# Performance work log

Hardware: AMD Instinct MI355X
Metric: run time of the kernel (lower is better)

## Reference

```python
import jax, jax.numpy as jnp
import numpy as np

B, IN_CH, OUT_CH = 4, 64, 128
N_HIGH, N_LOW = 163842, 40962
GROUPS, EPS, SLOPE = 4, 1e-5, 0.2


def setup_inputs() -> dict:
    key = jax.random.key(0)
    ks = jax.random.split(key, 6)
    x = jax.random.normal(ks[0], (B, IN_CH, N_HIGH), jnp.float32)
    pool_neigh = jax.random.randint(ks[1], (N_LOW * 7,), 0, N_HIGH, dtype=jnp.int32)
    conv_neigh = jax.random.randint(ks[2], (N_LOW * 7,), 0, N_LOW, dtype=jnp.int32)
    W1 = jax.random.normal(ks[3], (OUT_CH, 7 * IN_CH), jnp.float32) / np.float32(np.sqrt(7 * IN_CH))
    b1 = jnp.zeros((OUT_CH,), jnp.float32)
    W2 = jax.random.normal(ks[4], (OUT_CH, 7 * OUT_CH), jnp.float32) / np.float32(np.sqrt(7 * OUT_CH))
    b2 = jnp.zeros((OUT_CH,), jnp.float32)
    return dict(x=x, pool_neigh=pool_neigh, conv_neigh=conv_neigh,
                W1=W1, b1=b1, gn1_w=jnp.ones((OUT_CH,), jnp.float32), gn1_b=jnp.zeros((OUT_CH,), jnp.float32),
                W2=W2, b2=b2, gn2_w=jnp.ones((OUT_CH,), jnp.float32), gn2_b=jnp.zeros((OUT_CH,), jnp.float32))


def _mean_pool(x, pool_neigh):
    # x: (B, C, N_high); pool_neigh: (N_low*7,) -> (B, C, N_low)
    g = x[:, :, pool_neigh].reshape(x.shape[0], x.shape[1], -1, 7)
    return g.mean(axis=-1)


def _onering_conv(x, neigh, W, b):
    # x: (B, C, N); neigh: (N*7,); W: (O, 7*C). Torch Linear over gathered
    # (N*7, C).view(N, 7*C): neighbor-major, channel-minor concatenation.
    Bb, C, N = x.shape
    feat = x[:, :, neigh].reshape(Bb, C, N, 7)            # (B, C, N, 7)
    feat = jnp.transpose(feat, (0, 2, 3, 1)).reshape(Bb, N, 7 * C)  # (B, N, 7C)
    out = jnp.einsum('bnf,of->bno', feat, W) + b          # (B, N, O)
    return jnp.transpose(out, (0, 2, 1))                  # (B, O, N)


def _group_norm(x, w, b):
    # x: (B, C, N), normalize per (group, sample) over (C//G, N)
    Bb, C, N = x.shape
    xg = x.reshape(Bb, GROUPS, C // GROUPS, N)
    mu = xg.mean(axis=(2, 3), keepdims=True)
    var = ((xg - mu) ** 2).mean(axis=(2, 3), keepdims=True)
    xn = ((xg - mu) * jax.lax.rsqrt(var + EPS)).reshape(Bb, C, N)
    return xn * w[None, :, None] + b[None, :, None]


def _leaky_relu(x):
    return jnp.where(x >= 0, x, SLOPE * x)


def reference(x, pool_neigh, conv_neigh, W1, b1, gn1_w, gn1_b, W2, b2, gn2_w, gn2_b):
    h = _mean_pool(x, pool_neigh)
    h = _leaky_relu(_group_norm(_onering_conv(h, conv_neigh, W1, b1), gn1_w, gn1_b))
    h = _leaky_relu(_group_norm(_onering_conv(h, conv_neigh, W2, b2), gn2_w, gn2_b))
    return h
```

## Files before the change

### kernel.cpp

```cpp
#include <hip/hip_runtime.h>

#define B_SZ 4
#define IN_CH 64
#define OUT_CH 128
#define NHI 163842
#define NLO 40962
#define EPS_GN 1e-5f
#define SLOPE 0.2f

typedef __attribute__((ext_vector_type(8))) short short8;
typedef __attribute__((ext_vector_type(16))) float f32x16;

__device__ inline ushort f2bf(float f) {
    union { float f; unsigned u; } v; v.f = f;
    unsigned r = v.u + 0x7FFF + ((v.u >> 16) & 1);
    return (ushort)(r >> 16);
}
__device__ inline float bf2f(ushort h) {
    union { unsigned u; float f; } v; v.u = ((unsigned)h) << 16;
    return v.f;
}

__device__ inline void glds16(const ushort* g, ushort* l) {
    typedef __attribute__((address_space(1))) const void gv;
    typedef __attribute__((address_space(3))) void lv;
    __builtin_amdgcn_global_load_lds((gv*)g, (lv*)l, 16, 0, 0);
}

__global__ void k_transpose_x(const float* __restrict__ x, ushort* __restrict__ xT) {
    __shared__ float t[64][65];
    const int b   = blockIdx.y;
    const int n0  = blockIdx.x * 64;
    const int tid = threadIdx.x;
    const int nq  = tid & 15;
    const int c0  = tid >> 4;
    const bool full = (n0 + 64) <= NHI;
    if (full) {
#pragma unroll
        for (int r = 0; r < 4; ++r) {
            int c = c0 + r * 16;
            float4 v = *(const float4*)&x[((long)b * IN_CH + c) * NHI + n0 + nq * 4];
            t[c][nq * 4 + 0] = v.x; t[c][nq * 4 + 1] = v.y;
            t[c][nq * 4 + 2] = v.z; t[c][nq * 4 + 3] = v.w;
        }
    } else {
        for (int r = 0; r < 4; ++r) {
            int c = c0 + r * 16;
            for (int e = 0; e < 4; ++e) {
                int n = n0 + nq * 4 + e;
                t[c][nq * 4 + e] = (n < NHI) ? x[((long)b * IN_CH + c) * NHI + n] : 0.f;
            }
        }
    }
    __syncthreads();
    const int n  = tid >> 2;
    const int cc = (tid & 3) * 16;
    if (n0 + n < NHI) {
        short8 o0, o1;
#pragma unroll
        for (int e = 0; e < 8; ++e) {
            o0[e] = (short)f2bf(t[cc + e][n]);
            o1[e] = (short)f2bf(t[cc + 8 + e][n]);
        }
        ushort* p = &xT[((long)b * NHI + n0 + n) * 64 + cc];
        *(short8*)p = o0;
        *(short8*)(p + 8) = o1;
    }
}

__global__ void k_prep_w(const float* __restrict__ W, ushort* __restrict__ Wb, int K) {
    int i = blockIdx.x * 256 + threadIdx.x;
    if (i >= K * 128) return;
    int k = i / 128, o = i % 128;
    int step = k >> 6, kk = k & 63, kg = kk >> 3, e = kk & 7;
    Wb[(((long)(step * 8 + kg) * 128 + o) * 8) + e] = f2bf(W[(long)o * K + k]);
}

__global__ void k_pool(const ushort* __restrict__ xT, const int* __restrict__ pn,
                       ushort* __restrict__ h1) {
    long t = (long)blockIdx.x * 256 + threadIdx.x;
    const long total = (long)B_SZ * NLO * 8;
    if (t >= total) return;
    int  cq = (int)(t & 7);
    long bn = t >> 3;
    int  n  = (int)(bn % NLO);
    int  b  = (int)(bn / NLO);
    float acc[8] = {};
#pragma unroll
    for (int j = 0; j < 7; ++j) {
        int idx = pn[n * 7 + j];
        short8 v = *(const short8*)&xT[((long)b * NHI + idx) * 64 + cq * 8];
#pragma unroll
        for (int e = 0; e < 8; ++e) acc[e] += bf2f((ushort)v[e]);
    }
    short8 o;
#pragma unroll
    for (int e = 0; e < 8; ++e) o[e] = (short)f2bf(acc[e] * (1.f / 7.f));
    *(short8*)&h1[bn * 64 + cq * 8] = o;
}

template <int CIN>
__global__ __launch_bounds__(256, 2)
void k_conv_mfma(const ushort* __restrict__ src, const int* __restrict__ nbr,
                 const ushort* __restrict__ Wb, const float* __restrict__ bias,
                 ushort* __restrict__ out, float* __restrict__ part) {
    constexpr int NSTEP = 7 * CIN / 64;
    __shared__ ushort Asm[2][8192];
    __shared__ ushort Bsm[2][8192];
    __shared__ float  red[4][2][2];

    const int b     = blockIdx.y;
    const int n0    = blockIdx.x * 128;
    const int tid   = threadIdx.x;
    const int lane  = tid & 63;
    const int wave  = tid >> 6;
    const int wr    = wave >> 1, wc = wave & 1;
    const int l31   = lane & 31;
    const int khalf = lane >> 5;

    const int s_nn = tid >> 2;
    const int s_kq = tid & 3;
    const int r0 = min(n0 + s_nn, NLO - 1);
    const int r1 = min(n0 + 64 + s_nn, NLO - 1);
    int nb0[7], nb1[7];
#pragma unroll
    for (int j = 0; j < 7; ++j) {
        nb0[j] = nbr[r0 * 7 + j];
        nb1[j] = nbr[r1 * 7 + j];
    }

    const long srcb = (long)b * NLO * CIN;
    f32x16 acc[2][2] = {};
    short8 a00, a01, a10, a11;

#pragma unroll
    for (int i = 0; i < 4; ++i) {
        int off = (wave * 4 + i) * 512;
        glds16(&Wb[off + lane * 8], &Bsm[0][off]);
    }
    {
        const ushort* p0 = &src[srcb + (long)nb0[0] * CIN + s_kq * 8];
        const ushort* p1 = &src[srcb + (long)nb1[0] * CIN + s_kq * 8];
        a00 = *(const short8*)p0; a01 = *(const short8*)(p0 + 32);
        a10 = *(const short8*)p1; a11 = *(const short8*)(p1 + 32);
        *(short8*)&Asm[0][(s_kq * 128 + s_nn) * 8]            = a00;
        *(short8*)&Asm[0][((s_kq + 4) * 128 + s_nn) * 8]      = a01;
        *(short8*)&Asm[0][(s_kq * 128 + 64 + s_nn) * 8]       = a10;
        *(short8*)&Asm[0][((s_kq + 4) * 128 + 64 + s_nn) * 8] = a11;
    }
    __syncthreads();

    for (int step = 0; step < NSTEP; ++step) {
        const int cur = step & 1;
        const int nxt = cur ^ 1;
        if (step + 1 < NSTEP) {
#pragma unroll
            for (int i = 0; i < 4; ++i) {
                int off = (wave * 4 + i) * 512;
                glds16(&Wb[(long)(step + 1) * 8192 + off + lane * 8], &Bsm[nxt][off]);
            }
            const int s  = step + 1;
            const int j  = (CIN == 64) ? s : (s >> 1);
            const int cb = (CIN == 64) ? 0 : ((s & 1) * 64);
            const ushort* p0 = &src[srcb + (long)nb0[j] * CIN + cb + s_kq * 8];
            const ushort* p1 = &src[srcb + (long)nb1[j] * CIN + cb + s_kq * 8];
            a00 = *(const short8*)p0; a01 = *(const short8*)(p0 + 32);
            a10 = *(const short8*)p1; a11 = *(const short8*)(p1 + 32);
        }
#pragma unroll
        for (int kh = 0; kh < 4; ++kh) {
            const int kg = 2 * kh + khalf;
            short8 A0 = *(const short8*)&Asm[cur][(kg * 128 + wr * 64 + l31) * 8];
            short8 A1 = *(const short8*)&Asm[cur][(kg * 128 + wr * 64 + 32 + l31) * 8];
            short8 B0 = *(const short8*)&Bsm[cur][(kg * 128 + wc * 64 + l31) * 8];
            short8 B1 = *(const short8*)&Bsm[cur][(kg * 128 + wc * 64 + 32 + l31) * 8];
            acc[0][0] = __builtin_amdgcn_mfma_f32_32x32x16_bf16(A0, B0, acc[0][0], 0, 0, 0);
            acc[0][1] = __builtin_amdgcn_mfma_f32_32x32x16_bf16(A0, B1, acc[0][1], 0, 0, 0);
            acc[1][0] = __builtin_amdgcn_mfma_f32_32x32x16_bf16(A1, B0, acc[1][0], 0, 0, 0);
            acc[1][1] = __builtin_amdgcn_mfma_f32_32x32x16_bf16(A1, B1, acc[1][1], 0, 0, 0);
        }
        if (step + 1 < NSTEP) {
            *(short8*)&Asm[nxt][(s_kq * 128 + s_nn) * 8]            = a00;
            *(short8*)&Asm[nxt][((s_kq + 4) * 128 + s_nn) * 8]      = a01;
            *(short8*)&Asm[nxt][(s_kq * 128 + 64 + s_nn) * 8]       = a10;
            *(short8*)&Asm[nxt][((s_kq + 4) * 128 + 64 + s_nn) * 8] = a11;
        }
        __syncthreads();
    }

    float bia[2];
#pragma unroll
    for (int n = 0; n < 2; ++n) bia[n] = bias[wc * 64 + n * 32 + l31];
    float s[2] = {}, q[2] = {};
#pragma unroll
    for (int m = 0; m < 2; ++m)
#pragma unroll
        for (int n = 0; n < 2; ++n)
#pragma unroll
            for (int r = 0; r < 16; ++r) {
                int crow = (r & 3) + 8 * (r >> 2) + 4 * khalf;
                int row  = n0 + wr * 64 + m * 32 + crow;
                float v  = acc[m][n][r] + bia[n];
                if (row < NLO) {
                    out[((long)b * NLO + row) * 128 + wc * 64 + n * 32 + l31] = f2bf(v);
                    s[n] += v; q[n] += v * v;
                }
            }
#pragma unroll
    for (int n = 0; n < 2; ++n)
#pragma unroll
        for (int off = 32; off > 0; off >>= 1) {
            s[n] += __shfl_down(s[n], off);
            q[n] += __shfl_down(q[n], off);
        }
    if (lane == 0) {
#pragma unroll
        for (int n = 0; n < 2; ++n) { red[wave][n][0] = s[n]; red[wave][n][1] = q[n]; }
    }
    __syncthreads();
    if (tid < 8) {
        int g = tid >> 1, isq = tid & 1;
        int gwc = g >> 1, gn = g & 1;
        float v = red[gwc][gn][isq] + red[2 + gwc][gn][isq];
        part[(((long)b * gridDim.x + blockIdx.x) * 4 + g) * 2 + isq] = v;
    }
}

__global__ void k_finalize(const float* __restrict__ part, int nblk,
                           const float* __restrict__ w, const float* __restrict__ bb,
                           float* __restrict__ scale, float* __restrict__ shift) {
    const int b = blockIdx.x >> 2, g = blockIdx.x & 3;
    const int tid = threadIdx.x;
    float s = 0.f, ss = 0.f;
    for (int k = tid; k < nblk; k += 256) {
        s  += part[(((long)b * nblk + k) * 4 + g) * 2 + 0];
        ss += part[(((long)b * nblk + k) * 4 + g) * 2 + 1];
    }
#pragma unroll
    for (int off = 32; off > 0; off >>= 1) {
        s += __shfl_down(s, off); ss += __shfl_down(ss, off);
    }
    __shared__ float red[8];
    __shared__ float fin[2];
    const int wave = tid >> 6, lane = tid & 63;
    if (lane == 0) { red[wave * 2] = s; red[wave * 2 + 1] = ss; }
    __syncthreads();
    if (tid == 0) {
        float as = red[0] + red[2] + red[4] + red[6];
        float aq = red[1] + red[3] + red[5] + red[7];
        const float cnt = 32.f * NLO;
        float mu  = as / cnt;
        float var = aq / cnt - mu * mu;
        fin[0] = mu; fin[1] = rsqrtf(var + EPS_GN);
    }
    __syncthreads();
    if (tid < 32) {
        int c = g * 32 + tid;
        float sc = fin[1] * w[c];
        scale[b * 128 + c] = sc;
        shift[b * 128 + c] = bb[c] - fin[0] * sc;
    }
}

__global__ void k_gnapply(const ushort* __restrict__ y, const float* __restrict__ sc,
                          const float* __restrict__ sh, ushort* __restrict__ yp) {
    long t = (long)blockIdx.x * 256 + threadIdx.x;
    const long total = (long)B_SZ * NLO * 16;
    if (t >= total) return;
    int  c8 = (int)(t & 15);
    long bn = t >> 4;
    int  b  = (int)(bn / NLO);
    short8 v = *(const short8*)&y[bn * 128 + c8 * 8];
    short8 o;
#pragma unroll
    for (int e = 0; e < 8; ++e) {
        int c = c8 * 8 + e;
        float f = bf2f((ushort)v[e]) * sc[b * 128 + c] + sh[b * 128 + c];
        f = fmaxf(f, SLOPE * f);
        o[e] = (short)f2bf(f);
    }
    *(short8*)&yp[bn * 128 + c8 * 8] = o;
}

__global__ void k_output(const ushort* __restrict__ y2, const float* __restrict__ scale,
                         const float* __restrict__ shift, float* __restrict__ out) {
    __shared__ float t[32][129];
    const int b   = blockIdx.y;
    const int n0  = blockIdx.x * 32;
    const int tid = threadIdx.x;
    const float* scb = &scale[b * 128];
    const float* shb = &shift[b * 128];
    const int c8 = (tid & 15) * 8;
#pragma unroll
    for (int r = 0; r < 2; ++r) {
        int nn = (tid >> 4) + r * 16;
        int n  = n0 + nn;
        if (n < NLO) {
            short8 v = *(const short8*)&y2[((long)b * NLO + n) * 128 + c8];
#pragma unroll
            for (int e = 0; e < 8; ++e) {
                int c = c8 + e;
                float f = bf2f((ushort)v[e]) * scb[c] + shb[c];
                t[nn][c] = fmaxf(f, SLOPE * f);
            }
        } else {
#pragma unroll
            for (int e = 0; e < 8; ++e) t[nn][c8 + e] = 0.f;
        }
    }
    __syncthreads();
    const int n4 = (tid & 7) * 4;
    const bool full = (n0 + 32) <= NLO;
#pragma unroll
    for (int r = 0; r < 4; ++r) {
        int c = (tid >> 3) + r * 32;
        long o = ((long)b * 128 + c) * NLO + n0 + n4;
        if (full) {
            float2 v0 = make_float2(t[n4][c], t[n4 + 1][c]);
            float2 v1 = make_float2(t[n4 + 2][c], t[n4 + 3][c]);
            *(float2*)&out[o]     = v0;
            *(float2*)&out[o + 2] = v1;
        } else {
            for (int e = 0; e < 4; ++e)
                if (n0 + n4 + e < NLO) out[o + e] = t[n4 + e][c];
        }
    }
}

extern "C" void kernel_launch(void* const* d_in, const int* in_sizes, int n_in,
                              void* d_out, int out_size, void* d_ws, size_t ws_size,
                              hipStream_t stream) {
    const float* x   = (const float*)d_in[0];
    const int*   pn  = (const int*)d_in[1];
    const int*   cn  = (const int*)d_in[2];
    const float* W1  = (const float*)d_in[3];
    const float* b1  = (const float*)d_in[4];
    const float* g1w = (const float*)d_in[5];
    const float* g1b = (const float*)d_in[6];
    const float* W2  = (const float*)d_in[7];
    const float* b2  = (const float*)d_in[8];
    const float* g2w = (const float*)d_in[9];
    const float* g2b = (const float*)d_in[10];
    float* out = (float*)d_out;
    char*  base = (char*)d_ws;

    ushort* xT  = (ushort*)(base + 0);
    ushort* y1  = (ushort*)(base + 0);
    ushort* y1p = (ushort*)(base + 44000000);
    ushort* h1  = (ushort*)(base + 88000000);
    ushort* y2  = (ushort*)(base + 110000000);
    ushort* wb1 = (ushort*)(base + 152000000);
    ushort* wb2 = (ushort*)(base + 152200000);
    float*  p1  = (float*)(base + 152500000);
    float*  p2  = (float*)(base + 152600000);
    float*  sc1 = (float*)(base + 152700000);
    float*  sh1 = sc1 + 512;
    float*  sc2 = (float*)(base + 152710000);
    float*  sh2 = sc2 + 512;

    const int NBLK = (NLO + 127) / 128;

    k_transpose_x<<<dim3((NHI + 63) / 64, B_SZ), 256, 0, stream>>>(x, xT);
    k_prep_w<<<(448 * 128 + 255) / 256, 256, 0, stream>>>(W1, wb1, 448);
    k_prep_w<<<(896 * 128 + 255) / 256, 256, 0, stream>>>(W2, wb2, 896);
    k_pool<<<(int)(((long)B_SZ * NLO * 8 + 255) / 256), 256, 0, stream>>>(xT, pn, h1);
    k_conv_mfma<64><<<dim3(NBLK, B_SZ), 256, 0, stream>>>(h1, cn, wb1, b1, y1, p1);
    k_finalize<<<16, 256, 0, stream>>>(p1, NBLK, g1w, g1b, sc1, sh1);
    k_gnapply<<<(int)(((long)B_SZ * NLO * 16 + 255) / 256), 256, 0, stream>>>(y1, sc1, sh1, y1p);
    k_conv_mfma<128><<<dim3(NBLK, B_SZ), 256, 0, stream>>>(y1p, cn, wb2, b2, y2, p2);
    k_finalize<<<16, 256, 0, stream>>>(p2, NBLK, g2w, g2b, sc2, sh2);
    k_output<<<dim3((NLO + 31) / 32, B_SZ), 256, 0, stream>>>(y2, sc2, sh2, out);
}
```

Before: 276.6 us.

## Load conv weights directly into registers, swizzle A tile LDS, raise occupancy

The weight tile is no longer staged through shared memory with async global-to-LDS copies. Each wave now reads its MFMA B fragments straight from global memory (L2/L1-resident) into registers every step. This halves LDS usage, which together with launch bounds raised to 3 blocks per CU is meant to increase occupancy. An XOR swizzle on the gathered A tile layout aims to reduce LDS bank conflicts. The cost is that the weight loads are no longer prefetched a step ahead, so MFMAs may stall on global latency, and register pressure rises.

```diff
diff --git a/kernel.cpp b/kernel.cpp
--- a/kernel.cpp
+++ b/kernel.cpp
@@ -19,12 +19,6 @@
 __device__ inline float bf2f(ushort h) {
     union { unsigned u; float f; } v; v.u = ((unsigned)h) << 16;
     return v.f;
-}
-
-__device__ inline void glds16(const ushort* g, ushort* l) {
-    typedef __attribute__((address_space(1))) const void gv;
-    typedef __attribute__((address_space(3))) void lv;
-    __builtin_amdgcn_global_load_lds((gv*)g, (lv*)l, 16, 0, 0);
 }
 
 __global__ void k_transpose_x(const float* __restrict__ x, ushort* __restrict__ xT) {
@@ -99,14 +93,17 @@
     *(short8*)&h1[bn * 64 + cq * 8] = o;
 }
 
+__device__ inline int aidx(int kg, int nn) {
+    return (kg * 128 + (nn ^ (kg << 1))) * 8;
+}
+
 template <int CIN>
-__global__ __launch_bounds__(256, 2)
+__global__ __launch_bounds__(256, 3)
 void k_conv_mfma(const ushort* __restrict__ src, const int* __restrict__ nbr,
                  const ushort* __restrict__ Wb, const float* __restrict__ bias,
                  ushort* __restrict__ out, float* __restrict__ part) {
     constexpr int NSTEP = 7 * CIN / 64;
     __shared__ ushort Asm[2][8192];
-    __shared__ ushort Bsm[2][8192];
     __shared__ float  red[4][2][2];
 
     const int b     = blockIdx.y;
@@ -133,32 +130,31 @@
     f32x16 acc[2][2] = {};
     short8 a00, a01, a10, a11;
 
-#pragma unroll
-    for (int i = 0; i < 4; ++i) {
-        int off = (wave * 4 + i) * 512;
-        glds16(&Wb[off + lane * 8], &Bsm[0][off]);
-    }
     {
         const ushort* p0 = &src[srcb + (long)nb0[0] * CIN + s_kq * 8];
         const ushort* p1 = &src[srcb + (long)nb1[0] * CIN + s_kq * 8];
         a00 = *(const short8*)p0; a01 = *(const short8*)(p0 + 32);
         a10 = *(const short8*)p1; a11 = *(const short8*)(p1 + 32);
-        *(short8*)&Asm[0][(s_kq * 128 + s_nn) * 8]            = a00;
-        *(short8*)&Asm[0][((s_kq + 4) * 128 + s_nn) * 8]      = a01;
-        *(short8*)&Asm[0][(s_kq * 128 + 64 + s_nn) * 8]       = a10;
-        *(short8*)&Asm[0][((s_kq + 4) * 128 + 64 + s_nn) * 8] = a11;
+        *(short8*)&Asm[0][aidx(s_kq,     s_nn)]      = a00;
+        *(short8*)&Asm[0][aidx(s_kq + 4, s_nn)]      = a01;
+        *(short8*)&Asm[0][aidx(s_kq,     64 + s_nn)] = a10;
+        *(short8*)&Asm[0][aidx(s_kq + 4, 64 + s_nn)] = a11;
     }
     __syncthreads();
 
     for (int step = 0; step < NSTEP; ++step) {
         const int cur = step & 1;
         const int nxt = cur ^ 1;
+        short8 bfr[4][2];
+        {
+            const ushort* wb = &Wb[(long)step * 8192 + (khalf * 128 + wc * 64 + l31) * 8];
+#pragma unroll
+            for (int kh = 0; kh < 4; ++kh) {
+                bfr[kh][0] = *(const short8*)(wb + kh * 2 * 128 * 8);
+                bfr[kh][1] = *(const short8*)(wb + kh * 2 * 128 * 8 + 32 * 8);
+            }
+        }
         if (step + 1 < NSTEP) {
-#pragma unroll
-            for (int i = 0; i < 4; ++i) {
-                int off = (wave * 4 + i) * 512;
-                glds16(&Wb[(long)(step + 1) * 8192 + off + lane * 8], &Bsm[nxt][off]);
-            }
             const int s  = step + 1;
             const int j  = (CIN == 64) ? s : (s >> 1);
             const int cb = (CIN == 64) ? 0 : ((s & 1) * 64);
@@ -170,20 +166,18 @@
 #pragma unroll
         for (int kh = 0; kh < 4; ++kh) {
             const int kg = 2 * kh + khalf;
-            short8 A0 = *(const short8*)&Asm[cur][(kg * 128 + wr * 64 + l31) * 8];
-            short8 A1 = *(const short8*)&Asm[cur][(kg * 128 + wr * 64 + 32 + l31) * 8];
-            short8 B0 = *(const short8*)&Bsm[cur][(kg * 128 + wc * 64 + l31) * 8];
-            short8 B1 = *(const short8*)&Bsm[cur][(kg * 128 + wc * 64 + 32 + l31) * 8];
-            acc[0][0] = __builtin_amdgcn_mfma_f32_32x32x16_bf16(A0, B0, acc[0][0], 0, 0, 0);
-            acc[0][1] = __builtin_amdgcn_mfma_f32_32x32x16_bf16(A0, B1, acc[0][1], 0, 0, 0);
-            acc[1][0] = __builtin_amdgcn_mfma_f32_32x32x16_bf16(A1, B0, acc[1][0], 0, 0, 0);
-            acc[1][1] = __builtin_amdgcn_mfma_f32_32x32x16_bf16(A1, B1, acc[1][1], 0, 0, 0);
+            short8 A0 = *(const short8*)&Asm[cur][aidx(kg, wr * 64 + l31)];
+            short8 A1 = *(const short8*)&Asm[cur][aidx(kg, wr * 64 + 32 + l31)];
+            acc[0][0] = __builtin_amdgcn_mfma_f32_32x32x16_bf16(A0, bfr[kh][0], acc[0][0], 0, 0, 0);
+            acc[0][1] = __builtin_amdgcn_mfma_f32_32x32x16_bf16(A0, bfr[kh][1], acc[0][1], 0, 0, 0);
+            acc[1][0] = __builtin_amdgcn_mfma_f32_32x32x16_bf16(A1, bfr[kh][0], acc[1][0], 0, 0, 0);
+            acc[1][1] = __builtin_amdgcn_mfma_f32_32x32x16_bf16(A1, bfr[kh][1], acc[1][1], 0, 0, 0);
         }
         if (step + 1 < NSTEP) {
-            *(short8*)&Asm[nxt][(s_kq * 128 + s_nn) * 8]            = a00;
-            *(short8*)&Asm[nxt][((s_kq + 4) * 128 + s_nn) * 8]      = a01;
-            *(short8*)&Asm[nxt][(s_kq * 128 + 64 + s_nn) * 8]       = a10;
-            *(short8*)&Asm[nxt][((s_kq + 4) * 128 + 64 + s_nn) * 8] = a11;
+            *(short8*)&Asm[nxt][aidx(s_kq,     s_nn)]      = a00;
+            *(short8*)&Asm[nxt][aidx(s_kq + 4, s_nn)]      = a01;
+            *(short8*)&Asm[nxt][aidx(s_kq,     64 + s_nn)] = a10;
+            *(short8*)&Asm[nxt][aidx(s_kq + 4, 64 + s_nn)] = a11;
         }
         __syncthreads();
     }
```

After: 262.4 us. 1.05x faster.

## Swizzle A tile in LDS and restructure conv gather pipeline per row

Applied to the files above, without the earlier changes.

Applies an XOR swizzle to the A-tile LDS index to cut bank conflicts on MFMA operand reads. Each thread pair now gathers one node row (four contiguous 16-byte loads) instead of four threads per two rows, and neighbor indices are re-read from global memory each step instead of being held in registers. The pipeline is reordered so the A tile is written to LDS at the top of each step, followed by one barrier. The loop is fully unrolled. This frees registers and improves LDS access, but the global stores of the next tile now overlap less with MFMA work.

```diff
diff --git a/kernel.cpp b/kernel.cpp
--- a/kernel.cpp
+++ b/kernel.cpp
@@ -99,6 +99,10 @@
     *(short8*)&h1[bn * 64 + cq * 8] = o;
 }
 
+__device__ inline int aidx(int kg, int nn) {
+    return (kg * 128 + (nn ^ (kg << 1))) * 8;
+}
+
 template <int CIN>
 __global__ __launch_bounds__(256, 2)
 void k_conv_mfma(const ushort* __restrict__ src, const int* __restrict__ nbr,
@@ -118,60 +122,52 @@
     const int l31   = lane & 31;
     const int khalf = lane >> 5;
 
-    const int s_nn = tid >> 2;
-    const int s_kq = tid & 3;
-    const int r0 = min(n0 + s_nn, NLO - 1);
-    const int r1 = min(n0 + 64 + s_nn, NLO - 1);
-    int nb0[7], nb1[7];
-#pragma unroll
-    for (int j = 0; j < 7; ++j) {
-        nb0[j] = nbr[r0 * 7 + j];
-        nb1[j] = nbr[r1 * 7 + j];
-    }
+    const int s_nn = tid >> 1;
+    const int s_h  = tid & 1;
+    const int nrow = min(n0 + s_nn, NLO - 1);
+    const int* nbr_row = &nbr[nrow * 7];
 
     const long srcb = (long)b * NLO * CIN;
     f32x16 acc[2][2] = {};
-    short8 a00, a01, a10, a11;
-
-#pragma unroll
-    for (int i = 0; i < 4; ++i) {
-        int off = (wave * 4 + i) * 512;
-        glds16(&Wb[off + lane * 8], &Bsm[0][off]);
-    }
-    {
-        const ushort* p0 = &src[srcb + (long)nb0[0] * CIN + s_kq * 8];
-        const ushort* p1 = &src[srcb + (long)nb1[0] * CIN + s_kq * 8];
-        a00 = *(const short8*)p0; a01 = *(const short8*)(p0 + 32);
-        a10 = *(const short8*)p1; a11 = *(const short8*)(p1 + 32);
-        *(short8*)&Asm[0][(s_kq * 128 + s_nn) * 8]            = a00;
-        *(short8*)&Asm[0][((s_kq + 4) * 128 + s_nn) * 8]      = a01;
-        *(short8*)&Asm[0][(s_kq * 128 + 64 + s_nn) * 8]       = a10;
-        *(short8*)&Asm[0][((s_kq + 4) * 128 + 64 + s_nn) * 8] = a11;
-    }
-    __syncthreads();
-
+    short8 a[4];
+
+    auto loadA = [&](int t) {
+        int j, cb;
+        if (CIN == 64) { j = t; cb = 0; }
+        else           { j = t >> 1; cb = (t & 1) * 64; }
+        const ushort* sp = &src[srcb + (long)nbr_row[j] * CIN + cb + s_h * 32];
+#pragma unroll
+        for (int i = 0; i < 4; ++i) a[i] = *(const short8*)(sp + i * 8);
+    };
+    auto writeA = [&](int buf) {
+#pragma unroll
+        for (int i = 0; i < 4; ++i)
+            *(short8*)&Asm[buf][aidx(s_h * 4 + i, s_nn)] = a[i];
+    };
+    auto gldsB = [&](int t, int buf) {
+#pragma unroll
+        for (int i = 0; i < 4; ++i)
+            glds16(&Wb[(long)t * 8192 + (i * 256 + tid) * 8],
+                   &Bsm[buf][(i * 256 + tid) * 8]);
+    };
+
+    gldsB(0, 0);
+    loadA(0);
+
+#pragma unroll
     for (int step = 0; step < NSTEP; ++step) {
         const int cur = step & 1;
-        const int nxt = cur ^ 1;
+        writeA(cur);
+        __syncthreads();
         if (step + 1 < NSTEP) {
-#pragma unroll
-            for (int i = 0; i < 4; ++i) {
-                int off = (wave * 4 + i) * 512;
-                glds16(&Wb[(long)(step + 1) * 8192 + off + lane * 8], &Bsm[nxt][off]);
-            }
-            const int s  = step + 1;
-            const int j  = (CIN == 64) ? s : (s >> 1);
-            const int cb = (CIN == 64) ? 0 : ((s & 1) * 64);
-            const ushort* p0 = &src[srcb + (long)nb0[j] * CIN + cb + s_kq * 8];
-            const ushort* p1 = &src[srcb + (long)nb1[j] * CIN + cb + s_kq * 8];
-            a00 = *(const short8*)p0; a01 = *(const short8*)(p0 + 32);
-            a10 = *(const short8*)p1; a11 = *(const short8*)(p1 + 32);
+            gldsB(step + 1, cur ^ 1);
+            loadA(step + 1);
         }
 #pragma unroll
         for (int kh = 0; kh < 4; ++kh) {
             const int kg = 2 * kh + khalf;
-            short8 A0 = *(const short8*)&Asm[cur][(kg * 128 + wr * 64 + l31) * 8];
-            short8 A1 = *(const short8*)&Asm[cur][(kg * 128 + wr * 64 + 32 + l31) * 8];
+            short8 A0 = *(const short8*)&Asm[cur][aidx(kg, wr * 64 + l31)];
+            short8 A1 = *(const short8*)&Asm[cur][aidx(kg, wr * 64 + 32 + l31)];
             short8 B0 = *(const short8*)&Bsm[cur][(kg * 128 + wc * 64 + l31) * 8];
             short8 B1 = *(const short8*)&Bsm[cur][(kg * 128 + wc * 64 + 32 + l31) * 8];
             acc[0][0] = __builtin_amdgcn_mfma_f32_32x32x16_bf16(A0, B0, acc[0][0], 0, 0, 0);
@@ -179,13 +175,6 @@
             acc[1][0] = __builtin_amdgcn_mfma_f32_32x32x16_bf16(A1, B0, acc[1][0], 0, 0, 0);
             acc[1][1] = __builtin_amdgcn_mfma_f32_32x32x16_bf16(A1, B1, acc[1][1], 0, 0, 0);
         }
-        if (step + 1 < NSTEP) {
-            *(short8*)&Asm[nxt][(s_kq * 128 + s_nn) * 8]            = a00;
-            *(short8*)&Asm[nxt][((s_kq + 4) * 128 + s_nn) * 8]      = a01;
-            *(short8*)&Asm[nxt][(s_kq * 128 + 64 + s_nn) * 8]       = a10;
-            *(short8*)&Asm[nxt][((s_kq + 4) * 128 + 64 + s_nn) * 8] = a11;
-        }
-        __syncthreads();
     }
 
     float bia[2];
```

Result: faster. 268.1 us (-3.1%).
